# Performance work log

Hardware: AMD Instinct MI355X
Metric: run time of the kernel (lower is better)

Reference implementation:

```python
import jax, jax.numpy as jnp
import numpy as np

N = 100_000      # amino-acid nodes
E = 1_600_000    # edges per relation (avg degree 16)
D = 128          # input_dim
H = 128          # hidden_dim
L = 2            # num_layers
EPS = 1e-5       # BatchNorm eps


def setup_inputs() -> dict:
    key = jax.random.key(0)
    ks = jax.random.split(key, 20)
    inp = {
        "x": jax.random.normal(ks[0], (N, D), dtype=jnp.float32),
        "src_residue": jax.random.randint(ks[1], (E,), 0, N, dtype=jnp.int32),
        "dst_residue": jax.random.randint(ks[2], (E,), 0, N, dtype=jnp.int32),
        "src_seq": jax.random.randint(ks[3], (E,), 0, N, dtype=jnp.int32),
        "dst_seq": jax.random.randint(ks[4], (E,), 0, N, dtype=jnp.int32),
        "src_knn": jax.random.randint(ks[5], (E,), 0, N, dtype=jnp.int32),
        "dst_knn": jax.random.randint(ks[6], (E,), 0, N, dtype=jnp.int32),
        # GraphConv weights: 3 relations per layer; layer0 in=D, layer1 in=H
        "Wg0": jax.random.normal(ks[7], (3, D, H), dtype=jnp.float32) * (1.0 / np.sqrt(D)),
        "bg0": jnp.zeros((3, H), dtype=jnp.float32),
        "Wg1": jax.random.normal(ks[8], (3, H, H), dtype=jnp.float32) * (1.0 / np.sqrt(H)),
        "bg1": jnp.zeros((3, H), dtype=jnp.float32),
        # FC per layer
        "Wfc": jax.random.normal(ks[9], (L, H, H), dtype=jnp.float32) * (1.0 / np.sqrt(H)),
        "bfc": jax.random.normal(ks[10], (L, H), dtype=jnp.float32) * 0.01,
        # BatchNorm1d (eval mode: running stats)
        "bn_gamma": 1.0 + 0.1 * jax.random.normal(ks[11], (L, H), dtype=jnp.float32),
        "bn_beta": 0.1 * jax.random.normal(ks[12], (L, H), dtype=jnp.float32),
        "bn_mean": 0.1 * jax.random.normal(ks[13], (L, H), dtype=jnp.float32),
        "bn_var": jax.random.uniform(ks[14], (L, H), dtype=jnp.float32, minval=0.5, maxval=1.5),
    }
    return inp


def reference(x, src_residue, dst_residue, src_seq, dst_seq, src_knn, dst_knn,
              Wg0, bg0, Wg1, bg1, Wfc, bfc, bn_gamma, bn_beta, bn_mean, bn_var):
    n = x.shape[0]
    edges = [(src_residue, dst_residue), (src_seq, dst_seq), (src_knn, dst_knn)]

    def gconv(h, src, dst, W, b):
        # DGL GraphConv, norm='both': D_dst^{-1/2} A D_src^{-1/2} h W + b
        ones = jnp.ones(src.shape, h.dtype)
        deg_out = jnp.maximum(jax.ops.segment_sum(ones, src, num_segments=n), 1.0)
        deg_in = jnp.maximum(jax.ops.segment_sum(ones, dst, num_segments=n), 1.0)
        hn = h * jax.lax.rsqrt(deg_out)[:, None]
        agg = jax.ops.segment_sum(hn[src], dst, num_segments=n)  # [N, d] gather+scatter
        agg = agg * jax.lax.rsqrt(deg_in)[:, None]
        return agg @ W + b

    h = x
    layer_weights = [(Wg0, bg0), (Wg1, bg1)]
    for i, (Wg, bg) in enumerate(layer_weights):
        # HeteroGraphConv with aggregate='sum' over 3 relations
        out = gconv(h, edges[0][0], edges[0][1], Wg[0], bg[0])
        out = out + gconv(h, edges[1][0], edges[1][1], Wg[1], bg[1])
        out = out + gconv(h, edges[2][0], edges[2][1], Wg[2], bg[2])
        y = jax.nn.relu(out @ Wfc[i] + bfc[i])
        # BatchNorm1d (eval: running stats); dropout is identity in eval mode
        h = (y - bn_mean[i]) * jax.lax.rsqrt(bn_var[i] + EPS) * bn_gamma[i] + bn_beta[i]
    return h
```

## Files before the change

kernel.cpp:

```cpp
#include <hip/hip_runtime.h>
#include <stdint.h>

#define NN 100000
#define NE 1600000
#define NE4 (NE / 4)
#define NNP1 100008
#define NBK 196
#define NSL 64

typedef __attribute__((ext_vector_type(8))) short bfrag;
typedef __attribute__((ext_vector_type(4))) float ffrag;

__device__ __forceinline__ uint16_t f2bf(float f) {
  uint32_t u = __float_as_uint(f);
  u += 0x7fff + ((u >> 16) & 1);
  return (uint16_t)(u >> 16);
}
__device__ __forceinline__ uint32_t pack2(float a, float b) {
  return (uint32_t)f2bf(a) | ((uint32_t)f2bf(b) << 16);
}

__global__ void k_cast_x(const float* __restrict__ x, uint32_t* __restrict__ h) {
  int n = NN * 64;
  for (int i = blockIdx.x * blockDim.x + threadIdx.x; i < n; i += gridDim.x * blockDim.x) {
    float2 v = ((const float2*)x)[i];
    h[i] = pack2(v.x, v.y);
  }
}

__global__ void k_matmul_wc(const float* __restrict__ Wg0, const float* __restrict__ Wg1,
                            const float* __restrict__ Wfc, float* __restrict__ Wc) {
  int b = blockIdx.x;
  int m = b >> 2, kq = b & 3;
  int l = m / 3, rel = m % 3;
  int t = threadIdx.x;
  int n = t & 127, kh = t >> 7;
  int k0 = kq * 32 + kh * 16;
  const float* Wg = (l ? Wg1 : Wg0) + rel * 16384;
  const float* Wf = Wfc + (size_t)l * 16384;
  for (int k = k0; k < k0 + 16; k++) {
    float acc = 0.f;
    for (int kk = 0; kk < 128; kk++) acc = fmaf(Wg[k * 128 + kk], Wf[kk * 128 + n], acc);
    Wc[(size_t)m * 16384 + k * 128 + n] = acc;
  }
}

__global__ void k_prep_w(const float* __restrict__ Wc, uint16_t* __restrict__ wswz) {
  int idx = blockIdx.x * 256 + threadIdx.x;
  int rem = idx & 16383;
  int m = idx >> 14;
  int j = rem & 7;
  int lane = (rem >> 3) & 63;
  int f = rem >> 9;
  int t = f >> 3, ct = f & 7;
  int k = t * 32 + (lane >> 4) * 8 + j;
  int n = ct * 16 + (lane & 15);
  wswz[idx] = f2bf(Wc[(size_t)m * 16384 + k * 128 + n]);
}

__global__ void k_prep_consts(const float* __restrict__ bg0, const float* __restrict__ bg1,
                              const float* __restrict__ Wfc, const float* __restrict__ bfc,
                              const float* __restrict__ gamma, const float* __restrict__ beta,
                              const float* __restrict__ mean, const float* __restrict__ var,
                              float* __restrict__ cst) {
  int tid = threadIdx.x;
  int l = tid >> 7, n = tid & 127;
  const float* bg = l ? bg1 : bg0;
  float acc = bfc[l * 128 + n];
  for (int k = 0; k < 128; k++) {
    float bsum = bg[k] + bg[128 + k] + bg[256 + k];
    acc += bsum * Wfc[l * 16384 + k * 128 + n];
  }
  cst[tid] = acc;
  float g = gamma[tid] * rsqrtf(var[tid] + 1e-5f);
  cst[256 + tid] = g;
  cst[512 + tid] = beta[tid] - mean[tid] * g;
}

__global__ void k_bhist(const int* __restrict__ s0, const int* __restrict__ s1,
                        const int* __restrict__ s2, const int* __restrict__ d0,
                        const int* __restrict__ d1, const int* __restrict__ d2,
                        uint32_t* __restrict__ bh) {
  int r = blockIdx.y, blk = blockIdx.x, t = threadIdx.x;
  __shared__ uint32_t hD[NBK], hS[NBK];
  for (int i = t; i < NBK; i += 256) { hD[i] = 0; hS[i] = 0; }
  __syncthreads();
  const int4* sp = (const int4*)((r == 0) ? s0 : (r == 1) ? s1 : s2);
  const int4* dp = (const int4*)((r == 0) ? d0 : (r == 1) ? d1 : d2);
  int base = blk * (NE4 / NSL);
  for (int i = t; i < NE4 / NSL; i += 256) {
    int4 s = sp[base + i];
    int4 d = dp[base + i];
    atomicAdd(&hD[d.x >> 9], 1u); atomicAdd(&hD[d.y >> 9], 1u);
    atomicAdd(&hD[d.z >> 9], 1u); atomicAdd(&hD[d.w >> 9], 1u);
    atomicAdd(&hS[s.x >> 9], 1u); atomicAdd(&hS[s.y >> 9], 1u);
    atomicAdd(&hS[s.z >> 9], 1u); atomicAdd(&hS[s.w >> 9], 1u);
  }
  __syncthreads();
  for (int i = t; i < NBK; i += 256) {
    if (hD[i]) atomicAdd(&bh[r * NBK + i], hD[i]);
    if (hS[i]) atomicAdd(&bh[(3 + r) * NBK + i], hS[i]);
  }
}

__global__ void k_bscan(const uint32_t* __restrict__ bh, int* __restrict__ bases,
                        uint32_t* __restrict__ cur, int* __restrict__ rowptr) {
  int seg = blockIdx.x, t = threadIdx.x;
  int lane = t & 63, wid = t >> 6;
  int v = (t < NBK) ? (int)bh[seg * NBK + t] : 0;
  int x = v;
#pragma unroll
  for (int o = 1; o < 64; o <<= 1) { int y = __shfl_up(x, o); if (lane >= o) x += y; }
  __shared__ int ws[4];
  if (lane == 63) ws[wid] = x;
  __syncthreads();
  int woff = 0;
  for (int i = 0; i < wid; i++) woff += ws[i];
  int incl = woff + x, excl = incl - v;
  if (t < NBK) { bases[seg * (NBK + 1) + t] = excl; cur[seg * NBK + t] = (uint32_t)excl; }
  if (t == 255) bases[seg * (NBK + 1) + NBK] = incl;
  if (seg < 3 && t == 0) rowptr[seg * NNP1 + NN] = NE;
}

__global__ void k_bscatter(const int* __restrict__ s0, const int* __restrict__ s1,
                           const int* __restrict__ s2, const int* __restrict__ d0,
                           const int* __restrict__ d1, const int* __restrict__ d2,
                           uint32_t* __restrict__ cur, uint32_t* __restrict__ pairs,
                           uint16_t* __restrict__ srcs) {
  int r = blockIdx.y, blk = blockIdx.x, t = threadIdx.x;
  __shared__ uint32_t hD[NBK], hS[NBK];
  for (int i = t; i < NBK; i += 256) { hD[i] = 0; hS[i] = 0; }
  __syncthreads();
  const int4* sp = (const int4*)((r == 0) ? s0 : (r == 1) ? s1 : s2);
  const int4* dp = (const int4*)((r == 0) ? d0 : (r == 1) ? d1 : d2);
  int base = blk * (NE4 / NSL);
  for (int i = t; i < NE4 / NSL; i += 256) {
    int4 s = sp[base + i];
    int4 d = dp[base + i];
    atomicAdd(&hD[d.x >> 9], 1u); atomicAdd(&hD[d.y >> 9], 1u);
    atomicAdd(&hD[d.z >> 9], 1u); atomicAdd(&hD[d.w >> 9], 1u);
    atomicAdd(&hS[s.x >> 9], 1u); atomicAdd(&hS[s.y >> 9], 1u);
    atomicAdd(&hS[s.z >> 9], 1u); atomicAdd(&hS[s.w >> 9], 1u);
  }
  __syncthreads();
  for (int i = t; i < NBK; i += 256) {
    hD[i] = atomicAdd(&cur[r * NBK + i], hD[i]);
    hS[i] = atomicAdd(&cur[(3 + r) * NBK + i], hS[i]);
  }
  __syncthreads();
  uint32_t* pr = pairs + (size_t)r * NE;
  uint16_t* sr = srcs + (size_t)r * NE;
#define SCAT1(S, D) { \
    uint32_t p = atomicAdd(&hD[(D) >> 9], 1u); \
    pr[p] = (uint32_t)(((D) & 511) << 17) | (uint32_t)(S); \
    uint32_t q = atomicAdd(&hS[(S) >> 9], 1u); \
    sr[q] = (uint16_t)((S) & 511); }
  for (int i = t; i < NE4 / NSL; i += 256) {
    int4 s = sp[base + i];
    int4 d = dp[base + i];
    SCAT1(s.x, d.x) SCAT1(s.y, d.y) SCAT1(s.z, d.z) SCAT1(s.w, d.w)
  }
#undef SCAT1
}

__global__ void k_bucket_sout(const uint16_t* __restrict__ srcs, const int* __restrict__ bases,
                              float* __restrict__ s_out) {
  int b = blockIdx.x, r = blockIdx.y, t = threadIdx.x;
  int node0 = b << 9;
  int nc = min(512, NN - node0);
  int rb = bases[(3 + r) * (NBK + 1) + b];
  int m = bases[(3 + r) * (NBK + 1) + b + 1] - rb;
  __shared__ int cnt[512];
  cnt[t] = 0; cnt[t + 256] = 0;
  __syncthreads();
  const uint16_t* pp = srcs + (size_t)r * NE + rb;
  for (int i = t; i < m; i += 256) atomicAdd(&cnt[pp[i]], 1);
  __syncthreads();
  for (int i = t; i < nc; i += 256)
    s_out[r * NN + node0 + i] = rsqrtf((float)(cnt[i] < 1 ? 1 : cnt[i]));
}

__global__ void k_bucket_csr(const uint32_t* __restrict__ pairs, const int* __restrict__ bases,
                             const float* __restrict__ s_out, int* __restrict__ rowptr,
                             float* __restrict__ s_in, int2* __restrict__ col2) {
  int b = blockIdx.x, r = blockIdx.y, t = threadIdx.x;
  int node0 = b << 9;
  int nc = min(512, NN - node0);
  int rb = bases[r * (NBK + 1) + b];
  int m = bases[r * (NBK + 1) + b + 1] - rb;
  __shared__ int cnt[512];
  __shared__ int exc[512];
  __shared__ int ws[4];
  cnt[t] = 0; cnt[t + 256] = 0;
  __syncthreads();
  const uint32_t* pp = pairs + (size_t)r * NE + rb;
  for (int i = t; i < m; i += 256) atomicAdd(&cnt[pp[i] >> 17], 1);
  __syncthreads();
  int v0 = cnt[2 * t], v1 = cnt[2 * t + 1];
  int s = v0 + v1, x = s;
  int lane = t & 63, wid = t >> 6;
#pragma unroll
  for (int o = 1; o < 64; o <<= 1) { int y = __shfl_up(x, o); if (lane >= o) x += y; }
  if (lane == 63) ws[wid] = x;
  __syncthreads();
  int woff = 0;
  for (int i = 0; i < wid; i++) woff += ws[i];
  int e0 = woff + x - s;
  exc[2 * t] = e0;
  exc[2 * t + 1] = e0 + v0;
  __syncthreads();
  for (int i = t; i < nc; i += 256) {
    rowptr[r * NNP1 + node0 + i] = rb + exc[i];
    s_in[r * NN + node0 + i] = rsqrtf((float)(cnt[i] < 1 ? 1 : cnt[i]));
  }
  __syncthreads();
  int2* cl = col2 + (size_t)r * NE + rb;
  for (int i = t; i < m; i += 256) {
    uint32_t e = pp[i];
    int src = (int)(e & 0x1FFFF);
    int p = atomicAdd(&exc[e >> 17], 1);
    cl[p] = make_int2(src, __float_as_int(s_out[r * NN + src]));
  }
}

__global__ void k_aggregate(const uint32_t* __restrict__ h, const int* __restrict__ rowptr,
                            const int2* __restrict__ col2, const float* __restrict__ s_in,
                            uint32_t* __restrict__ agg) {
  int r = blockIdx.y;
  int node = blockIdx.x * 4 + (threadIdx.x >> 6);
  int lane = threadIdx.x & 63;
  const int* rp = rowptr + r * NNP1;
  int beg = rp[node], end = rp[node + 1];
  const int2* cl = col2 + (size_t)r * NE;
  float a0 = 0.f, a1 = 0.f;
  for (int base = beg; base < end; base += 64) {
    int idx = base + lane;
    int sv = 0; int wb = 0;
    if (idx < end) { int2 e = cl[idx]; sv = e.x; wb = e.y; }
    int cnt = min(64, end - base);
    int cnt8 = (cnt + 7) & ~7;
    for (int j = 0; j < cnt8; j += 8) {
      uint32_t hv[8]; float ww[8];
#pragma unroll
      for (int u = 0; u < 8; u++) {
        int ss = __builtin_amdgcn_readlane(sv, j + u);
        ww[u] = __int_as_float(__builtin_amdgcn_readlane(wb, j + u));
        hv[u] = h[(size_t)ss * 64 + lane];
      }
#pragma unroll
      for (int u = 0; u < 8; u++) {
        a0 = fmaf(__uint_as_float(hv[u] << 16), ww[u], a0);
        a1 = fmaf(__uint_as_float(hv[u] & 0xffff0000u), ww[u], a1);
      }
    }
  }
  float sc = s_in[r * NN + node];
  agg[((size_t)r * NN + node) * 64 + lane] = pack2(a0 * sc, a1 * sc);
}

__global__ __launch_bounds__(256, 2) void k_fc2(const uint32_t* __restrict__ agg,
                                                const short* __restrict__ wswz,
                                                const float* __restrict__ cst, int l,
                                                uint16_t* __restrict__ hout,
                                                float* __restrict__ fout, int wf32) {
  int lane = threadIdx.x & 63;
  int wid = threadIdx.x >> 6;
  int q = lane >> 4, n0 = lane & 15;
  const bfrag* wb = (const bfrag*)(wswz + (size_t)(l * 3) * 16384);
  float bb[8], gg[8], b2v[8];
#pragma unroll
  for (int ct = 0; ct < 8; ct++) {
    int c = l * 128 + ct * 16 + n0;
    bb[ct] = cst[c];
    gg[ct] = cst[256 + c];
    b2v[ct] = cst[512 + c];
  }
  const int ntiles = NN / 32;
  for (int tile = blockIdx.x * 4 + wid; tile < ntiles; tile += gridDim.x * 4) {
    ffrag acc[2][8];
#pragma unroll
    for (int s = 0; s < 2; s++)
#pragma unroll
      for (int ct = 0; ct < 8; ct++) acc[s][ct] = (ffrag){0.f, 0.f, 0.f, 0.f};
    for (int kt = 0; kt < 12; kt++) {
      int rel = kt >> 2, kt4 = kt & 3;
      const uint32_t* A = agg + (size_t)rel * NN * 64 + kt4 * 16 + q * 4;
      bfrag a[2];
#pragma unroll
      for (int s = 0; s < 2; s++)
        a[s] = *(const bfrag*)(A + (size_t)(tile * 32 + s * 16 + n0) * 64);
      const bfrag* wk = wb + (size_t)rel * 2048 + (kt4 * 8) * 64 + lane;
#pragma unroll
      for (int ct = 0; ct < 8; ct++) {
        bfrag B = wk[ct * 64];
        acc[0][ct] = __builtin_amdgcn_mfma_f32_16x16x32_bf16(a[0], B, acc[0][ct], 0, 0, 0);
        acc[1][ct] = __builtin_amdgcn_mfma_f32_16x16x32_bf16(a[1], B, acc[1][ct], 0, 0, 0);
      }
    }
#pragma unroll
    for (int s = 0; s < 2; s++) {
      int orow = tile * 32 + s * 16 + q * 4;
#pragma unroll
      for (int ct = 0; ct < 8; ct++) {
#pragma unroll
        for (int i = 0; i < 4; i++) {
          float y = acc[s][ct][i] + bb[ct];
          y = fmaxf(y, 0.f);
          float hv = fmaf(y, gg[ct], b2v[ct]);
          size_t oi = (size_t)(orow + i) * 128 + ct * 16 + n0;
          if (wf32) fout[oi] = hv;
          else hout[oi] = f2bf(hv);
        }
      }
    }
  }
}

extern "C" void kernel_launch(void* const* d_in, const int* in_sizes, int n_in,
                              void* d_out, int out_size, void* d_ws, size_t ws_size,
                              hipStream_t stream) {
  const float* x = (const float*)d_in[0];
  const int* s0 = (const int*)d_in[1]; const int* d0 = (const int*)d_in[2];
  const int* s1 = (const int*)d_in[3]; const int* d1 = (const int*)d_in[4];
  const int* s2 = (const int*)d_in[5]; const int* d2 = (const int*)d_in[6];
  const float* Wg0 = (const float*)d_in[7];
  const float* bg0 = (const float*)d_in[8];
  const float* Wg1 = (const float*)d_in[9];
  const float* bg1 = (const float*)d_in[10];
  const float* Wfc = (const float*)d_in[11];
  const float* bfc = (const float*)d_in[12];
  const float* gamma = (const float*)d_in[13];
  const float* beta = (const float*)d_in[14];
  const float* mean = (const float*)d_in[15];
  const float* var = (const float*)d_in[16];

  char* ws = (char*)d_ws;
  size_t off = 0;
  auto alloc = [&](size_t bytes) { size_t o = off; off = (off + bytes + 255) & ~(size_t)255; return o; };
  size_t o_bh    = alloc((size_t)6 * NBK * 4);
  size_t o_bases = alloc((size_t)6 * (NBK + 1) * 4);
  size_t o_cur   = alloc((size_t)6 * NBK * 4);
  size_t o_sin   = alloc((size_t)3 * NN * 4);
  size_t o_sout  = alloc((size_t)3 * NN * 4);
  size_t o_rp    = alloc((size_t)3 * NNP1 * 4);
  size_t o_col2  = alloc((size_t)3 * NE * 8);
  size_t o_wc    = alloc((size_t)6 * 16384 * 4);
  size_t o_wswz  = alloc((size_t)6 * 16384 * 2);
  size_t o_cst   = alloc((size_t)768 * 4);
  size_t o_h     = alloc((size_t)NN * 128 * 2);
  size_t o_agg   = alloc((size_t)3 * NN * 128 * 2);
  (void)ws_size; (void)in_sizes; (void)n_in; (void)out_size;

  uint32_t* bh   = (uint32_t*)(ws + o_bh);
  int* bases     = (int*)(ws + o_bases);
  uint32_t* cur  = (uint32_t*)(ws + o_cur);
  float* s_in    = (float*)(ws + o_sin);
  float* s_out   = (float*)(ws + o_sout);
  int* rowptr    = (int*)(ws + o_rp);
  int2* col2     = (int2*)(ws + o_col2);
  float* Wc      = (float*)(ws + o_wc);
  uint16_t* wswz = (uint16_t*)(ws + o_wswz);
  float* cst     = (float*)(ws + o_cst);
  uint32_t* h    = (uint32_t*)(ws + o_h);
  uint32_t* agg  = (uint32_t*)(ws + o_agg);
  uint32_t* pairs = (uint32_t*)(ws + o_agg);
  uint16_t* srcs  = (uint16_t*)(ws + o_agg + (size_t)3 * NE * 4);

  hipMemsetAsync(ws + o_bh, 0, (size_t)6 * NBK * 4, stream);

  k_cast_x<<<2048, 256, 0, stream>>>(x, h);
  k_matmul_wc<<<24, 256, 0, stream>>>(Wg0, Wg1, Wfc, Wc);
  k_prep_w<<<384, 256, 0, stream>>>(Wc, wswz);
  k_prep_consts<<<1, 256, 0, stream>>>(bg0, bg1, Wfc, bfc, gamma, beta, mean, var, cst);
  k_bhist<<<dim3(NSL, 3), 256, 0, stream>>>(s0, s1, s2, d0, d1, d2, bh);
  k_bscan<<<6, 256, 0, stream>>>(bh, bases, cur, rowptr);
  k_bscatter<<<dim3(NSL, 3), 256, 0, stream>>>(s0, s1, s2, d0, d1, d2, cur, pairs, srcs);
  k_bucket_sout<<<dim3(NBK, 3), 256, 0, stream>>>(srcs, bases, s_out);
  k_bucket_csr<<<dim3(NBK, 3), 256, 0, stream>>>(pairs, bases, s_out, rowptr, s_in, col2);

  for (int l = 0; l < 2; l++) {
    k_aggregate<<<dim3(25000, 3), 256, 0, stream>>>(h, rowptr, col2, s_in, agg);
    k_fc2<<<256, 256, 0, stream>>>(agg, (const short*)wswz, cst, l,
                                   (uint16_t*)h, (float*)d_out, l);
  }
}
```

Baseline: 850.2 us.

## Use scalar edge loads in aggregate and 64-row tiles in fused FC

The aggregate kernel makes the node index wave-uniform, so edge entries (src, weight) load as uniform scalar loads per edge. This replaces the per-lane vector load plus readlane broadcast, and a scalar tail loop handles leftover edges. The FC kernel grows each wave's tile from 32 to 64 rows, so each weight fragment feeds four MFMAs instead of two, with bounds guards for the ragged last tile and a larger grid. The trade-offs are more accumulator registers, which may lower occupancy, and serialized scalar loads on high-degree nodes.

```diff
diff --git a/kernel.cpp b/kernel.cpp
--- a/kernel.cpp
+++ b/kernel.cpp
@@ -227,32 +227,33 @@
                             const int2* __restrict__ col2, const float* __restrict__ s_in,
                             uint32_t* __restrict__ agg) {
   int r = blockIdx.y;
-  int node = blockIdx.x * 4 + (threadIdx.x >> 6);
+  int node = __builtin_amdgcn_readfirstlane(blockIdx.x * 4 + (threadIdx.x >> 6));
   int lane = threadIdx.x & 63;
   const int* rp = rowptr + r * NNP1;
   int beg = rp[node], end = rp[node + 1];
   const int2* cl = col2 + (size_t)r * NE;
   float a0 = 0.f, a1 = 0.f;
-  for (int base = beg; base < end; base += 64) {
-    int idx = base + lane;
-    int sv = 0; int wb = 0;
-    if (idx < end) { int2 e = cl[idx]; sv = e.x; wb = e.y; }
-    int cnt = min(64, end - base);
-    int cnt8 = (cnt + 7) & ~7;
-    for (int j = 0; j < cnt8; j += 8) {
-      uint32_t hv[8]; float ww[8];
-#pragma unroll
-      for (int u = 0; u < 8; u++) {
-        int ss = __builtin_amdgcn_readlane(sv, j + u);
-        ww[u] = __int_as_float(__builtin_amdgcn_readlane(wb, j + u));
-        hv[u] = h[(size_t)ss * 64 + lane];
-      }
-#pragma unroll
-      for (int u = 0; u < 8; u++) {
-        a0 = fmaf(__uint_as_float(hv[u] << 16), ww[u], a0);
-        a1 = fmaf(__uint_as_float(hv[u] & 0xffff0000u), ww[u], a1);
-      }
+  int j = beg;
+  for (; j + 8 <= end; j += 8) {
+    uint32_t hv[8]; float ww[8];
+#pragma unroll
+    for (int u = 0; u < 8; u++) {
+      int2 e = cl[j + u];
+      ww[u] = __int_as_float(e.y);
+      hv[u] = h[(size_t)e.x * 64 + lane];
     }
+#pragma unroll
+    for (int u = 0; u < 8; u++) {
+      a0 = fmaf(__uint_as_float(hv[u] << 16), ww[u], a0);
+      a1 = fmaf(__uint_as_float(hv[u] & 0xffff0000u), ww[u], a1);
+    }
+  }
+  for (; j < end; j++) {
+    int2 e = cl[j];
+    uint32_t hv = h[(size_t)e.x * 64 + lane];
+    float w = __int_as_float(e.y);
+    a0 = fmaf(__uint_as_float(hv << 16), w, a0);
+    a1 = fmaf(__uint_as_float(hv & 0xffff0000u), w, a1);
   }
   float sc = s_in[r * NN + node];
   agg[((size_t)r * NN + node) * 64 + lane] = pack2(a0 * sc, a1 * sc);
@@ -275,41 +276,47 @@
     gg[ct] = cst[256 + c];
     b2v[ct] = cst[512 + c];
   }
-  const int ntiles = NN / 32;
+  const int ntiles = (NN + 63) / 64;
   for (int tile = blockIdx.x * 4 + wid; tile < ntiles; tile += gridDim.x * 4) {
-    ffrag acc[2][8];
-#pragma unroll
-    for (int s = 0; s < 2; s++)
+    ffrag acc[4][8];
+#pragma unroll
+    for (int s = 0; s < 4; s++)
 #pragma unroll
       for (int ct = 0; ct < 8; ct++) acc[s][ct] = (ffrag){0.f, 0.f, 0.f, 0.f};
     for (int kt = 0; kt < 12; kt++) {
       int rel = kt >> 2, kt4 = kt & 3;
       const uint32_t* A = agg + (size_t)rel * NN * 64 + kt4 * 16 + q * 4;
-      bfrag a[2];
-#pragma unroll
-      for (int s = 0; s < 2; s++)
-        a[s] = *(const bfrag*)(A + (size_t)(tile * 32 + s * 16 + n0) * 64);
+      bfrag a[4];
+#pragma unroll
+      for (int s = 0; s < 4; s++) {
+        int row = tile * 64 + s * 16 + n0;
+        row = row < NN ? row : 0;
+        a[s] = *(const bfrag*)(A + (size_t)row * 64);
+      }
       const bfrag* wk = wb + (size_t)rel * 2048 + (kt4 * 8) * 64 + lane;
 #pragma unroll
       for (int ct = 0; ct < 8; ct++) {
         bfrag B = wk[ct * 64];
-        acc[0][ct] = __builtin_amdgcn_mfma_f32_16x16x32_bf16(a[0], B, acc[0][ct], 0, 0, 0);
-        acc[1][ct] = __builtin_amdgcn_mfma_f32_16x16x32_bf16(a[1], B, acc[1][ct], 0, 0, 0);
+#pragma unroll
+        for (int s = 0; s < 4; s++)
+          acc[s][ct] = __builtin_amdgcn_mfma_f32_16x16x32_bf16(a[s], B, acc[s][ct], 0, 0, 0);
       }
     }
 #pragma unroll
-    for (int s = 0; s < 2; s++) {
-      int orow = tile * 32 + s * 16 + q * 4;
+    for (int s = 0; s < 4; s++) {
+      int orow = tile * 64 + s * 16 + q * 4;
 #pragma unroll
       for (int ct = 0; ct < 8; ct++) {
 #pragma unroll
         for (int i = 0; i < 4; i++) {
-          float y = acc[s][ct][i] + bb[ct];
-          y = fmaxf(y, 0.f);
-          float hv = fmaf(y, gg[ct], b2v[ct]);
-          size_t oi = (size_t)(orow + i) * 128 + ct * 16 + n0;
-          if (wf32) fout[oi] = hv;
-          else hout[oi] = f2bf(hv);
+          if (orow + i < NN) {
+            float y = acc[s][ct][i] + bb[ct];
+            y = fmaxf(y, 0.f);
+            float hv = fmaf(y, gg[ct], b2v[ct]);
+            size_t oi = (size_t)(orow + i) * 128 + ct * 16 + n0;
+            if (wf32) fout[oi] = hv;
+            else hout[oi] = f2bf(hv);
+          }
         }
       }
     }
@@ -380,7 +387,7 @@
 
   for (int l = 0; l < 2; l++) {
     k_aggregate<<<dim3(25000, 3), 256, 0, stream>>>(h, rowptr, col2, s_in, agg);
-    k_fc2<<<256, 256, 0, stream>>>(agg, (const short*)wswz, cst, l,
+    k_fc2<<<391, 256, 0, stream>>>(agg, (const short*)wswz, cst, l,
                                    (uint16_t*)h, (float*)d_out, l);
   }
 }
```

After: 1.011 ms. +19.0%, slower.

## Fuse neighbor aggregation with FC/BN epilogue and shrink CSR column entries

Applied to the files above, without the earlier changes.

Merges the per-relation gather-aggregate kernel and the MFMA FC/ReLU/BatchNorm kernel into one kernel per layer. Each block aggregates 16 nodes across all three relations into shared memory, then runs the bf16 MFMA on that tile, so the large intermediate aggregate buffer is never written to or read back from global memory. CSR column entries go from an int2 (source plus normalization) to a single int, and the source normalization is gathered from a small per-node array during aggregation. In exchange, each wave now processes 12 node-relations one after another, which may give less latency hiding than one node per wave, and each block re-reads the weight fragments.

```diff
diff --git a/kernel.cpp b/kernel.cpp
--- a/kernel.cpp
+++ b/kernel.cpp
@@ -7,6 +7,7 @@
 #define NNP1 100008
 #define NBK 196
 #define NSL 64
+#define APAD 196
 
 typedef __attribute__((ext_vector_type(8))) short bfrag;
 typedef __attribute__((ext_vector_type(4))) float ffrag;
@@ -163,6 +164,48 @@
 #undef SCAT1
 }
 
+__global__ void k_bucket_csr(const uint32_t* __restrict__ pairs, const int* __restrict__ bases,
+                             int* __restrict__ rowptr, float* __restrict__ s_in,
+                             int* __restrict__ col) {
+  int b = blockIdx.x, r = blockIdx.y, t = threadIdx.x;
+  int node0 = b << 9;
+  int nc = min(512, NN - node0);
+  int rb = bases[r * (NBK + 1) + b];
+  int m = bases[r * (NBK + 1) + b + 1] - rb;
+  __shared__ int cnt[512];
+  __shared__ int exc[512];
+  __shared__ int ws[4];
+  cnt[t] = 0; cnt[t + 256] = 0;
+  __syncthreads();
+  const uint32_t* pp = pairs + (size_t)r * NE + rb;
+  for (int i = t; i < m; i += 256) atomicAdd(&cnt[pp[i] >> 17], 1);
+  __syncthreads();
+  int v0 = cnt[2 * t], v1 = cnt[2 * t + 1];
+  int s = v0 + v1, x = s;
+  int lane = t & 63, wid = t >> 6;
+#pragma unroll
+  for (int o = 1; o < 64; o <<= 1) { int y = __shfl_up(x, o); if (lane >= o) x += y; }
+  if (lane == 63) ws[wid] = x;
+  __syncthreads();
+  int woff = 0;
+  for (int i = 0; i < wid; i++) woff += ws[i];
+  int e0 = woff + x - s;
+  exc[2 * t] = e0;
+  exc[2 * t + 1] = e0 + v0;
+  __syncthreads();
+  for (int i = t; i < nc; i += 256) {
+    rowptr[r * NNP1 + node0 + i] = rb + exc[i];
+    s_in[r * NN + node0 + i] = rsqrtf((float)(cnt[i] < 1 ? 1 : cnt[i]));
+  }
+  __syncthreads();
+  int* cl = col + (size_t)r * NE + rb;
+  for (int i = t; i < m; i += 256) {
+    uint32_t e = pp[i];
+    int p = atomicAdd(&exc[e >> 17], 1);
+    cl[p] = (int)(e & 0x1FFFF);
+  }
+}
+
 __global__ void k_bucket_sout(const uint16_t* __restrict__ srcs, const int* __restrict__ bases,
                               float* __restrict__ s_out) {
   int b = blockIdx.x, r = blockIdx.y, t = threadIdx.x;
@@ -180,138 +223,81 @@
     s_out[r * NN + node0 + i] = rsqrtf((float)(cnt[i] < 1 ? 1 : cnt[i]));
 }
 
-__global__ void k_bucket_csr(const uint32_t* __restrict__ pairs, const int* __restrict__ bases,
-                             const float* __restrict__ s_out, int* __restrict__ rowptr,
-                             float* __restrict__ s_in, int2* __restrict__ col2) {
-  int b = blockIdx.x, r = blockIdx.y, t = threadIdx.x;
-  int node0 = b << 9;
-  int nc = min(512, NN - node0);
-  int rb = bases[r * (NBK + 1) + b];
-  int m = bases[r * (NBK + 1) + b + 1] - rb;
-  __shared__ int cnt[512];
-  __shared__ int exc[512];
-  __shared__ int ws[4];
-  cnt[t] = 0; cnt[t + 256] = 0;
-  __syncthreads();
-  const uint32_t* pp = pairs + (size_t)r * NE + rb;
-  for (int i = t; i < m; i += 256) atomicAdd(&cnt[pp[i] >> 17], 1);
-  __syncthreads();
-  int v0 = cnt[2 * t], v1 = cnt[2 * t + 1];
-  int s = v0 + v1, x = s;
-  int lane = t & 63, wid = t >> 6;
-#pragma unroll
-  for (int o = 1; o < 64; o <<= 1) { int y = __shfl_up(x, o); if (lane >= o) x += y; }
-  if (lane == 63) ws[wid] = x;
-  __syncthreads();
-  int woff = 0;
-  for (int i = 0; i < wid; i++) woff += ws[i];
-  int e0 = woff + x - s;
-  exc[2 * t] = e0;
-  exc[2 * t + 1] = e0 + v0;
-  __syncthreads();
-  for (int i = t; i < nc; i += 256) {
-    rowptr[r * NNP1 + node0 + i] = rb + exc[i];
-    s_in[r * NN + node0 + i] = rsqrtf((float)(cnt[i] < 1 ? 1 : cnt[i]));
-  }
-  __syncthreads();
-  int2* cl = col2 + (size_t)r * NE + rb;
-  for (int i = t; i < m; i += 256) {
-    uint32_t e = pp[i];
-    int src = (int)(e & 0x1FFFF);
-    int p = atomicAdd(&exc[e >> 17], 1);
-    cl[p] = make_int2(src, __float_as_int(s_out[r * NN + src]));
-  }
-}
-
-__global__ void k_aggregate(const uint32_t* __restrict__ h, const int* __restrict__ rowptr,
-                            const int2* __restrict__ col2, const float* __restrict__ s_in,
-                            uint32_t* __restrict__ agg) {
-  int r = blockIdx.y;
-  int node = blockIdx.x * 4 + (threadIdx.x >> 6);
-  int lane = threadIdx.x & 63;
-  const int* rp = rowptr + r * NNP1;
-  int beg = rp[node], end = rp[node + 1];
-  const int2* cl = col2 + (size_t)r * NE;
-  float a0 = 0.f, a1 = 0.f;
-  for (int base = beg; base < end; base += 64) {
-    int idx = base + lane;
-    int sv = 0; int wb = 0;
-    if (idx < end) { int2 e = cl[idx]; sv = e.x; wb = e.y; }
-    int cnt = min(64, end - base);
-    int cnt8 = (cnt + 7) & ~7;
-    for (int j = 0; j < cnt8; j += 8) {
-      uint32_t hv[8]; float ww[8];
-#pragma unroll
-      for (int u = 0; u < 8; u++) {
-        int ss = __builtin_amdgcn_readlane(sv, j + u);
-        ww[u] = __int_as_float(__builtin_amdgcn_readlane(wb, j + u));
-        hv[u] = h[(size_t)ss * 64 + lane];
-      }
-#pragma unroll
-      for (int u = 0; u < 8; u++) {
-        a0 = fmaf(__uint_as_float(hv[u] << 16), ww[u], a0);
-        a1 = fmaf(__uint_as_float(hv[u] & 0xffff0000u), ww[u], a1);
-      }
-    }
-  }
-  float sc = s_in[r * NN + node];
-  agg[((size_t)r * NN + node) * 64 + lane] = pack2(a0 * sc, a1 * sc);
-}
-
-__global__ __launch_bounds__(256, 2) void k_fc2(const uint32_t* __restrict__ agg,
+__global__ __launch_bounds__(256) void k_agg_fc(const uint32_t* __restrict__ h,
+                                                const int* __restrict__ rowptr,
+                                                const int* __restrict__ col,
+                                                const float* __restrict__ s_out,
+                                                const float* __restrict__ s_in,
                                                 const short* __restrict__ wswz,
                                                 const float* __restrict__ cst, int l,
                                                 uint16_t* __restrict__ hout,
                                                 float* __restrict__ fout, int wf32) {
-  int lane = threadIdx.x & 63;
-  int wid = threadIdx.x >> 6;
-  int q = lane >> 4, n0 = lane & 15;
-  const bfrag* wb = (const bfrag*)(wswz + (size_t)(l * 3) * 16384);
-  float bb[8], gg[8], b2v[8];
-#pragma unroll
-  for (int ct = 0; ct < 8; ct++) {
-    int c = l * 128 + ct * 16 + n0;
-    bb[ct] = cst[c];
-    gg[ct] = cst[256 + c];
-    b2v[ct] = cst[512 + c];
-  }
-  const int ntiles = NN / 32;
-  for (int tile = blockIdx.x * 4 + wid; tile < ntiles; tile += gridDim.x * 4) {
-    ffrag acc[2][8];
-#pragma unroll
-    for (int s = 0; s < 2; s++)
-#pragma unroll
-      for (int ct = 0; ct < 8; ct++) acc[s][ct] = (ffrag){0.f, 0.f, 0.f, 0.f};
-    for (int kt = 0; kt < 12; kt++) {
-      int rel = kt >> 2, kt4 = kt & 3;
-      const uint32_t* A = agg + (size_t)rel * NN * 64 + kt4 * 16 + q * 4;
-      bfrag a[2];
-#pragma unroll
-      for (int s = 0; s < 2; s++)
-        a[s] = *(const bfrag*)(A + (size_t)(tile * 32 + s * 16 + n0) * 64);
-      const bfrag* wk = wb + (size_t)rel * 2048 + (kt4 * 8) * 64 + lane;
-#pragma unroll
-      for (int ct = 0; ct < 8; ct++) {
-        bfrag B = wk[ct * 64];
-        acc[0][ct] = __builtin_amdgcn_mfma_f32_16x16x32_bf16(a[0], B, acc[0][ct], 0, 0, 0);
-        acc[1][ct] = __builtin_amdgcn_mfma_f32_16x16x32_bf16(a[1], B, acc[1][ct], 0, 0, 0);
+  __shared__ uint32_t A[16 * APAD];
+  int base = blockIdx.x * 16;
+  int tid = threadIdx.x;
+  int wid = tid >> 6, lane = tid & 63;
+  for (int t = wid * 12; t < wid * 12 + 12; t++) {
+    int rel = t >> 4, ni = t & 15;
+    int node = base + ni;
+    const int* rp = rowptr + rel * NNP1;
+    int beg = rp[node], end = rp[node + 1];
+    const int* cl = col + (size_t)rel * NE;
+    const float* so = s_out + rel * NN;
+    float a0 = 0.f, a1 = 0.f;
+    for (int bs = beg; bs < end; bs += 64) {
+      int idx = bs + lane;
+      int sv = 0, wb = 0;
+      if (idx < end) { sv = cl[idx]; wb = __float_as_int(so[sv]); }
+      int cnt = min(64, end - bs);
+      int cnt8 = (cnt + 7) & ~7;
+      for (int j = 0; j < cnt8; j += 8) {
+        uint32_t hv[8]; float ww[8];
+#pragma unroll
+        for (int u = 0; u < 8; u++) {
+          int ss = __builtin_amdgcn_readlane(sv, j + u);
+          ww[u] = __int_as_float(__builtin_amdgcn_readlane(wb, j + u));
+          hv[u] = h[(size_t)ss * 64 + lane];
+        }
+#pragma unroll
+        for (int u = 0; u < 8; u++) {
+          a0 = fmaf(__uint_as_float(hv[u] << 16), ww[u], a0);
+          a1 = fmaf(__uint_as_float(hv[u] & 0xffff0000u), ww[u], a1);
+        }
       }
     }
-#pragma unroll
-    for (int s = 0; s < 2; s++) {
-      int orow = tile * 32 + s * 16 + q * 4;
-#pragma unroll
-      for (int ct = 0; ct < 8; ct++) {
-#pragma unroll
-        for (int i = 0; i < 4; i++) {
-          float y = acc[s][ct][i] + bb[ct];
-          y = fmaxf(y, 0.f);
-          float hv = fmaf(y, gg[ct], b2v[ct]);
-          size_t oi = (size_t)(orow + i) * 128 + ct * 16 + n0;
-          if (wf32) fout[oi] = hv;
-          else hout[oi] = f2bf(hv);
-        }
-      }
+    float sc = s_in[rel * NN + node];
+    A[ni * APAD + rel * 64 + lane] = pack2(a0 * sc, a1 * sc);
+  }
+  __syncthreads();
+  int q = lane >> 4, n0 = lane & 15;
+  ffrag acc[2] = {(ffrag){0.f,0.f,0.f,0.f}, (ffrag){0.f,0.f,0.f,0.f}};
+  const bfrag* wb2 = (const bfrag*)(wswz + (size_t)(l * 3) * 16384);
+  for (int kt = 0; kt < 12; kt++) {
+    int rel = kt >> 2, kt4 = kt & 3;
+    bfrag a = *(const bfrag*)(&A[n0 * APAD + rel * 64 + kt4 * 16 + q * 4]);
+    const bfrag* wk = wb2 + (size_t)rel * 2048 + (size_t)(kt4 * 8) * 64 + lane;
+#pragma unroll
+    for (int c = 0; c < 2; c++) {
+      bfrag B = wk[(size_t)(wid * 2 + c) * 64];
+      acc[c] = __builtin_amdgcn_mfma_f32_16x16x32_bf16(a, B, acc[c], 0, 0, 0);
+    }
+  }
+#pragma unroll
+  for (int c = 0; c < 2; c++) {
+    int ct = wid * 2 + c;
+    int colid = ct * 16 + n0;
+    float bb = cst[l * 128 + colid];
+    float gg = cst[256 + l * 128 + colid];
+    float b2 = cst[512 + l * 128 + colid];
+#pragma unroll
+    for (int i = 0; i < 4; i++) {
+      int row = base + q * 4 + i;
+      float y = acc[c][i] + bb;
+      y = fmaxf(y, 0.f);
+      float hv = fmaf(y, gg, b2);
+      size_t oi = (size_t)row * 128 + colid;
+      if (wf32) fout[oi] = hv;
+      else hout[oi] = f2bf(hv);
     }
   }
 }
@@ -343,12 +329,14 @@
   size_t o_sin   = alloc((size_t)3 * NN * 4);
   size_t o_sout  = alloc((size_t)3 * NN * 4);
   size_t o_rp    = alloc((size_t)3 * NNP1 * 4);
-  size_t o_col2  = alloc((size_t)3 * NE * 8);
+  size_t o_col   = alloc((size_t)3 * NE * 4);
   size_t o_wc    = alloc((size_t)6 * 16384 * 4);
   size_t o_wswz  = alloc((size_t)6 * 16384 * 2);
   size_t o_cst   = alloc((size_t)768 * 4);
   size_t o_h     = alloc((size_t)NN * 128 * 2);
-  size_t o_agg   = alloc((size_t)3 * NN * 128 * 2);
+  size_t o_h2    = alloc((size_t)NN * 128 * 2);
+  size_t o_pairs = alloc((size_t)3 * NE * 4);
+  size_t o_srcs  = alloc((size_t)3 * NE * 2);
   (void)ws_size; (void)in_sizes; (void)n_in; (void)out_size;
 
   uint32_t* bh   = (uint32_t*)(ws + o_bh);
@@ -357,14 +345,14 @@
   float* s_in    = (float*)(ws + o_sin);
   float* s_out   = (float*)(ws + o_sout);
   int* rowptr    = (int*)(ws + o_rp);
-  int2* col2     = (int2*)(ws + o_col2);
+  int* col       = (int*)(ws + o_col);
   float* Wc      = (float*)(ws + o_wc);
   uint16_t* wswz = (uint16_t*)(ws + o_wswz);
   float* cst     = (float*)(ws + o_cst);
   uint32_t* h    = (uint32_t*)(ws + o_h);
-  uint32_t* agg  = (uint32_t*)(ws + o_agg);
-  uint32_t* pairs = (uint32_t*)(ws + o_agg);
-  uint16_t* srcs  = (uint16_t*)(ws + o_agg + (size_t)3 * NE * 4);
+  uint32_t* h2   = (uint32_t*)(ws + o_h2);
+  uint32_t* pairs = (uint32_t*)(ws + o_pairs);
+  uint16_t* srcs  = (uint16_t*)(ws + o_srcs);
 
   hipMemsetAsync(ws + o_bh, 0, (size_t)6 * NBK * 4, stream);
 
@@ -375,12 +363,13 @@
   k_bhist<<<dim3(NSL, 3), 256, 0, stream>>>(s0, s1, s2, d0, d1, d2, bh);
   k_bscan<<<6, 256, 0, stream>>>(bh, bases, cur, rowptr);
   k_bscatter<<<dim3(NSL, 3), 256, 0, stream>>>(s0, s1, s2, d0, d1, d2, cur, pairs, srcs);
+  k_bucket_csr<<<dim3(NBK, 3), 256, 0, stream>>>(pairs, bases, rowptr, s_in, col);
   k_bucket_sout<<<dim3(NBK, 3), 256, 0, stream>>>(srcs, bases, s_out);
-  k_bucket_csr<<<dim3(NBK, 3), 256, 0, stream>>>(pairs, bases, s_out, rowptr, s_in, col2);
-
-  for (int l = 0; l < 2; l++) {
-    k_aggregate<<<dim3(25000, 3), 256, 0, stream>>>(h, rowptr, col2, s_in, agg);
-    k_fc2<<<256, 256, 0, stream>>>(agg, (const short*)wswz, cst, l,
-                                   (uint16_t*)h, (float*)d_out, l);
-  }
-}
+
+  k_agg_fc<<<6250, 256, 0, stream>>>(h, rowptr, col, s_out, s_in,
+                                     (const short*)wswz, cst, 0,
+                                     (uint16_t*)h2, (float*)d_out, 0);
+  k_agg_fc<<<6250, 256, 0, stream>>>(h2, rowptr, col, s_out, s_in,
+                                     (const short*)wswz, cst, 1,
+                                     (uint16_t*)h2, (float*)d_out, 1);
+}
```

Result: faster. 768.1 us (-9.7%).
